# Kernel tuning notes

Hardware: AMD Instinct MI355X
Metric: run time of the kernel (lower is better)

The kernel has to match this reference:

```python
import jax, jax.numpy as jnp
import numpy as np
import math

B, S, D = 16, 2048, 128
MASK_SENTINEL = -100

def setup_inputs() -> dict:
    key = jax.random.key(0)
    k1, k2, k3, k4 = jax.random.split(key, 4)
    value = jax.random.normal(k1, (B, S, D), dtype=jnp.float32)
    key_t = jax.random.normal(k2, (B, S, D), dtype=jnp.float32)
    query = jax.random.normal(k3, (B, S, D), dtype=jnp.float32)
    # mask uses -100 as the "masked out" sentinel, anything else is kept.
    bits = jax.random.randint(k4, (B, S, S), 0, 2, dtype=jnp.int32)
    mask = jnp.where(bits == 0, jnp.int32(MASK_SENTINEL), jnp.int32(0))
    return {"value": value, "key": key_t, "query": query, "mask": mask}

def reference(value, key, query, mask):
    # scores: [B, Sq, Sk]
    scale = 1.0 / math.sqrt(query.shape[-1])
    scores = jnp.einsum("bqd,bkd->bqk", query, key) * scale
    min_val = jnp.finfo(scores.dtype).min
    masked = jnp.where(mask == MASK_SENTINEL, min_val, scores)
    attn = jax.nn.softmax(masked, axis=-1)
    return jnp.einsum("bqk,bkd->bqd", attn, value)
```

## Files before the change

kernel.cpp:

```cpp
#include <hip/hip_runtime.h>
#include <hip/hip_bf16.h>

#define BATCH 16
#define SEQ   2048
#define DIM   128
#define QBLK  64
#define KVBLK 64
#define NT    (SEQ / KVBLK)
#define PPAD  72
#define L2E   1.4426950408889634f
#define THR   8.0f
#define MSENT -100

typedef __attribute__((ext_vector_type(8))) short bf16x8;
typedef __attribute__((ext_vector_type(4))) float f32x4;
typedef __attribute__((ext_vector_type(4))) int   i32x4;
typedef __attribute__((ext_vector_type(4))) unsigned u32x4;

__device__ __forceinline__ unsigned short f2bf(float f) {
  union { float f; unsigned u; } v; v.f = f;
  return (unsigned short)((v.u + 0x7FFFu + ((v.u >> 16) & 1u)) >> 16);
}
__device__ __forceinline__ unsigned packbf(float a, float b) {
  return ((unsigned)f2bf(b) << 16) | (unsigned)f2bf(a);
}

__global__ __launch_bounds__(256) void cvt_k(const float* __restrict__ K,
                                             short* __restrict__ Kb) {
  const size_t i = ((size_t)blockIdx.x * 256 + threadIdx.x) * 8;
  f32x4 a = __builtin_nontemporal_load((const f32x4*)(K + i));
  f32x4 b = __builtin_nontemporal_load((const f32x4*)(K + i + 4));
  u32x4 o = { packbf(a[0], a[1]), packbf(a[2], a[3]),
              packbf(b[0], b[1]), packbf(b[2], b[3]) };
  *(u32x4*)(Kb + i) = o;
}

__global__ __launch_bounds__(256) void cvt_vt(const float* __restrict__ V,
                                              short* __restrict__ Vt) {
  __shared__ unsigned t32[64][65];
  const int tid = threadIdx.x;
  const int b  = blockIdx.x >> 5;
  const int s0 = (blockIdx.x & 31) * 64;
  #pragma unroll
  for (int it = 0; it < 8; ++it) {
    const int idx = tid + it * 256;
    const int r = idx >> 5, c4 = idx & 31;
    f32x4 x = __builtin_nontemporal_load(
        (const f32x4*)(V + ((size_t)b * SEQ + s0 + r) * DIM + c4 * 4));
    t32[r][c4 * 2]     = packbf(x[0], x[1]);
    t32[r][c4 * 2 + 1] = packbf(x[2], x[3]);
  }
  __syncthreads();
  const int d = tid >> 1, sh = tid & 1;
  unsigned short outv[32];
  #pragma unroll
  for (int j = 0; j < 32; ++j) {
    const unsigned u = t32[sh * 32 + j][d >> 1];
    outv[j] = (d & 1) ? (unsigned short)(u >> 16) : (unsigned short)(u & 0xffff);
  }
  short* op = Vt + ((size_t)b * DIM + d) * SEQ + s0 + sh * 32;
  #pragma unroll
  for (int q = 0; q < 4; ++q) {
    bf16x8 y;
    #pragma unroll
    for (int j = 0; j < 8; ++j) y[j] = (short)outv[q * 8 + j];
    *(bf16x8*)(op + q * 8) = y;
  }
}

__device__ __forceinline__ void gload16(const void* g, void* l) {
  __builtin_amdgcn_global_load_lds(
      (const __attribute__((address_space(1))) unsigned*)g,
      (__attribute__((address_space(3))) unsigned*)l, 16, 0, 0);
}

__device__ __forceinline__ void stage_k(const char* __restrict__ Kb2,
                                        int k0, int w, int l, void* kbuf) {
  #pragma unroll
  for (int it = 0; it < 4; ++it) {
    const int ch = w * 4 + it;
    const int r  = ch * 4 + (l >> 4);
    const int sg = (l & 15) ^ (r & 15);
    gload16(Kb2 + (size_t)(k0 + r) * 256 + sg * 16, (char*)kbuf + ch * 1024);
  }
}
__device__ __forceinline__ void stage_v(const char* __restrict__ Vtb2,
                                        int k0, int w, int l, void* vbuf) {
  #pragma unroll
  for (int it = 0; it < 4; ++it) {
    const int ch = w * 4 + it;
    const int d2 = ch * 4 + (l >> 4);
    const int Su = (l & 15) ^ (d2 & 15);
    const int d  = 2 * d2 + (Su >> 3);
    const int m  = Su & 7;
    gload16(Vtb2 + (size_t)d * (SEQ * 2) + (size_t)k0 * 2 + m * 16,
            (char*)vbuf + ch * 1024);
  }
}

#define TILE_BODY(T, PAR, SA, SB, MA, MB)                                      \
  {                                                                            \
    if ((T) + 2 < NT) stage_k(Kb2, ((T) + 2) * KVBLK, w, l, lds_k[(PAR)]);     \
    if ((T) + 1 < NT) stage_v(Vtb2, ((T) + 1) * KVBLK, w, l, lds_v[(PAR) ^ 1]);\
    __builtin_amdgcn_sched_barrier(0);                                         \
                  \
    _Pragma("unroll") for (int sub = 0; sub < 4; ++sub)                        \
        _Pragma("unroll") for (int i = 0; i < 4; ++i)                          \
            if (MA[sub][i] == MSENT) SA[sub][i] = -1e30f;                      \
    {                                                                          \
      float tm = -1e30f;                                                       \
      _Pragma("unroll") for (int sub = 0; sub < 4; ++sub)                      \
          _Pragma("unroll") for (int i = 0; i < 4; ++i)                        \
              tm = fmaxf(tm, SA[sub][i]);                                      \
      tm = fmaxf(tm, __shfl_xor(tm, 16));                                      \
      tm = fmaxf(tm, __shfl_xor(tm, 32));                                      \
      if (__any(tm > mrow + THR)) {                                            \
        const float mnew = fmaxf(mrow, tm);                                    \
        const float al = __builtin_amdgcn_exp2f((mrow - mnew) * L2E);          \
        mrow = mnew; lsum *= al;                                               \
        float av[4];                                                           \
        _Pragma("unroll") for (int i = 0; i < 4; ++i)                          \
            av[i] = __shfl(al, 4 * g + i);                                     \
        _Pragma("unroll") for (int t8 = 0; t8 < 8; ++t8)                       \
            _Pragma("unroll") for (int i = 0; i < 4; ++i)                      \
                acc[t8][i] *= av[i];                                           \
      }                                                                        \
    }                                                                          \
           \
    if ((T) + 1 < NT) {                                                        \
      _Pragma("unroll") for (int sub = 0; sub < 4; ++sub)                      \
          MB[sub] = __builtin_nontemporal_load(                                \
              (const i32x4*)(Mr + ((T) + 1) * KVBLK + 16 * sub + 4 * g));      \
    }                                                                          \
               \
    if ((T) + 1 < NT) {                                                        \
      const char* kb_ = (const char*)lds_k[(PAR) ^ 1];                         \
      _Pragma("unroll") for (int sub = 0; sub < 4; ++sub)                      \
          SB[sub] = (f32x4){0.f, 0.f, 0.f, 0.f};                               \
      __builtin_amdgcn_s_setprio(1);                                           \
      _Pragma("unroll") for (int kk = 0; kk < 4; ++kk) {                       \
        const int cb = (64 * kk + 16 * g) ^ (lr << 4);                         \
        _Pragma("unroll") for (int sub = 0; sub < 4; ++sub) {                  \
          bf16x8 kb = *(const bf16x8*)(kb_ + (sub * 16 + lr) * 256 + cb);      \
          SB[sub] = __builtin_amdgcn_mfma_f32_16x16x32_bf16(kb, qa[kk],        \
                                                            SB[sub], 0, 0, 0); \
        }                                                                      \
      }                                                                        \
      __builtin_amdgcn_s_setprio(0);                                           \
    }                                                                          \
                               \
    {                                                                          \
      unsigned* prow = (unsigned*)&lds_p[w][lr * PPAD];                        \
      _Pragma("unroll") for (int sub = 0; sub < 4; ++sub) {                    \
        const float p0 = __builtin_amdgcn_exp2f((SA[sub][0] - mrow) * L2E);    \
        const float p1 = __builtin_amdgcn_exp2f((SA[sub][1] - mrow) * L2E);    \
        const float p2 = __builtin_amdgcn_exp2f((SA[sub][2] - mrow) * L2E);    \
        const float p3 = __builtin_amdgcn_exp2f((SA[sub][3] - mrow) * L2E);    \
        lsum += (p0 + p1) + (p2 + p3);                                         \
        prow[8 * sub + 2 * g]     = packbf(p0, p1);                            \
        prow[8 * sub + 2 * g + 1] = packbf(p2, p3);                            \
      }                                                                        \
      bf16x8 pa0 = *(const bf16x8*)&lds_p[w][lr * PPAD + g * 8];               \
      bf16x8 pa1 = *(const bf16x8*)&lds_p[w][lr * PPAD + 32 + g * 8];          \
      const char* vb_ = (const char*)lds_v[(PAR)];                             \
      __builtin_amdgcn_s_setprio(1);                                           \
      _Pragma("unroll") for (int t8 = 0; t8 < 8; ++t8) {                       \
        const int d2 = 8 * t8 + (lr >> 1);                                     \
        const int S0 = (((lr & 1) * 8 + 0 + g) ^ (d2 & 15)) * 16;              \
        const int S1 = (((lr & 1) * 8 + 4 + g) ^ (d2 & 15)) * 16;              \
        bf16x8 v0 = *(const bf16x8*)(vb_ + d2 * 256 + S0);                     \
        acc[t8] = __builtin_amdgcn_mfma_f32_16x16x32_bf16(pa0, v0, acc[t8],    \
                                                          0, 0, 0);            \
        bf16x8 v1 = *(const bf16x8*)(vb_ + d2 * 256 + S1);                     \
        acc[t8] = __builtin_amdgcn_mfma_f32_16x16x32_bf16(pa1, v1, acc[t8],    \
                                                          0, 0, 0);            \
      }                                                                        \
      __builtin_amdgcn_s_setprio(0);                                           \
    }                                                                          \
    if ((T) + 1 < NT) __syncthreads();                                         \
  }

__global__ __launch_bounds__(256, 2) void attn_fwd(
    const short* __restrict__ Kbf, const short* __restrict__ Vt,
    const float* __restrict__ Qg, const int* __restrict__ Mg,
    float* __restrict__ Og) {
  __shared__ short lds_k[2][KVBLK * DIM];
  __shared__ short lds_v[2][DIM * KVBLK];
  __shared__ short lds_p[4][16 * PPAD];

  const int tid = threadIdx.x;
  const int w = tid >> 6, l = tid & 63, g = l >> 4, lr = l & 15;

  const int blk = blockIdx.x;
  const int swz = (blk & 7) * 64 + (blk >> 3);
  const int b   = swz >> 5;
  const int q0  = (swz & 31) * QBLK;

  const float scale = 0.08838834764831845f;

  const char* Kb2  = (const char*)(Kbf + (size_t)b * SEQ * DIM);
  const char* Vtb2 = (const char*)(Vt  + (size_t)b * DIM * SEQ);
  const int*  Mr   = Mg + (size_t)b * SEQ * SEQ + (size_t)(q0 + w * 16 + lr) * SEQ;

  stage_k(Kb2, 0,     w, l, lds_k[0]);
  stage_k(Kb2, KVBLK, w, l, lds_k[1]);
  stage_v(Vtb2, 0,    w, l, lds_v[0]);
  __builtin_amdgcn_sched_barrier(0);
  i32x4 mA[4], mB[4];
  #pragma unroll
  for (int sub = 0; sub < 4; ++sub)
    mA[sub] = __builtin_nontemporal_load((const i32x4*)(Mr + 16 * sub + 4 * g));

  bf16x8 qa[4];
  {
    const float* qbase = Qg + ((size_t)b * SEQ + (size_t)(q0 + w * 16 + lr)) * DIM + g * 8;
    #pragma unroll
    for (int kk = 0; kk < 4; ++kk) {
      f32x4 x0 = *(const f32x4*)(qbase + kk * 32);
      f32x4 x1 = *(const f32x4*)(qbase + kk * 32 + 4);
      bf16x8 f;
      #pragma unroll
      for (int j = 0; j < 4; ++j) {
        f[j]     = (short)f2bf(x0[j] * scale);
        f[j + 4] = (short)f2bf(x1[j] * scale);
      }
      qa[kk] = f;
    }
  }

  f32x4 acc[8];
  #pragma unroll
  for (int t = 0; t < 8; ++t) acc[t] = (f32x4){0.f, 0.f, 0.f, 0.f};
  float mrow = -1e30f, lsum = 0.f;

  __syncthreads();

  f32x4 sA[4], sB[4];
  #pragma unroll
  for (int sub = 0; sub < 4; ++sub) sA[sub] = (f32x4){0.f, 0.f, 0.f, 0.f};
  {
    const char* kb_ = (const char*)lds_k[0];
    #pragma unroll
    for (int kk = 0; kk < 4; ++kk) {
      const int cb = (64 * kk + 16 * g) ^ (lr << 4);
      #pragma unroll
      for (int sub = 0; sub < 4; ++sub) {
        bf16x8 kb = *(const bf16x8*)(kb_ + (sub * 16 + lr) * 256 + cb);
        sA[sub] = __builtin_amdgcn_mfma_f32_16x16x32_bf16(kb, qa[kk], sA[sub], 0, 0, 0);
      }
    }
  }
  __syncthreads();

  for (int t = 0; t < NT; t += 2) {
    TILE_BODY(t,     0, sA, sB, mA, mB);
    TILE_BODY(t + 1, 1, sB, sA, mB, mA);
  }

  lsum += __shfl_xor(lsum, 16);
  lsum += __shfl_xor(lsum, 32);
  const float rden = 1.f / lsum;
  float rdv[4];
  #pragma unroll
  for (int i = 0; i < 4; ++i) rdv[i] = __shfl(rden, 4 * g + i);
  float* ob = Og + ((size_t)b * SEQ + (size_t)(q0 + w * 16)) * DIM;
  #pragma unroll
  for (int t8 = 0; t8 < 8; ++t8)
    #pragma unroll
    for (int i = 0; i < 4; ++i)
      ob[(4 * g + i) * DIM + 16 * t8 + lr] = acc[t8][i] * rdv[i];
}

extern "C" void kernel_launch(void* const* d_in, const int* in_sizes, int n_in,
                              void* d_out, int out_size, void* d_ws, size_t ws_size,
                              hipStream_t stream) {
  (void)in_sizes; (void)n_in; (void)out_size; (void)ws_size;
  const float* Vg = (const float*)d_in[0];
  const float* Kg = (const float*)d_in[1];
  const float* Qg = (const float*)d_in[2];
  const int*   Mg = (const int*)d_in[3];
  float* Og = (float*)d_out;

  short* Kbf = (short*)d_ws;
  short* Vt  = Kbf + (size_t)BATCH * SEQ * DIM;
  cvt_k<<<dim3(BATCH * SEQ * DIM / (8 * 256)), 256, 0, stream>>>(Kg, Kbf);
  cvt_vt<<<dim3(BATCH * (SEQ / 64)), 256, 0, stream>>>(Vg, Vt);
  attn_fwd<<<dim3(BATCH * (SEQ / QBLK)), 256, 0, stream>>>(Kbf, Vt, Qg, Mg, Og);
}
```

Measured before the change: 108.4 us.

## Load V tiles directly from global into registers instead of staging through LDS

Removes the LDS double-buffer for V. Each wave now reads its V^T fragments straight from global memory into 16 bf16x8 registers at the start of each tile, and the mask prefetch moves up next to those loads. This drops the LDS traffic and LDS footprint for V, which may allow higher occupancy. The costs are 64 extra VGPRs per thread, redundant global/L2 reads of the same V tile by all four waves, and V load latency that is no longer prefetched a tile ahead.

```diff
diff --git a/kernel.cpp b/kernel.cpp
--- a/kernel.cpp
+++ b/kernel.cpp
@@ -84,24 +84,21 @@
     gload16(Kb2 + (size_t)(k0 + r) * 256 + sg * 16, (char*)kbuf + ch * 1024);
   }
 }
-__device__ __forceinline__ void stage_v(const char* __restrict__ Vtb2,
-                                        int k0, int w, int l, void* vbuf) {
-  #pragma unroll
-  for (int it = 0; it < 4; ++it) {
-    const int ch = w * 4 + it;
-    const int d2 = ch * 4 + (l >> 4);
-    const int Su = (l & 15) ^ (d2 & 15);
-    const int d  = 2 * d2 + (Su >> 3);
-    const int m  = Su & 7;
-    gload16(Vtb2 + (size_t)d * (SEQ * 2) + (size_t)k0 * 2 + m * 16,
-            (char*)vbuf + ch * 1024);
-  }
-}
 
 #define TILE_BODY(T, PAR, SA, SB, MA, MB)                                      \
   {                                                                            \
     if ((T) + 2 < NT) stage_k(Kb2, ((T) + 2) * KVBLK, w, l, lds_k[(PAR)]);     \
-    if ((T) + 1 < NT) stage_v(Vtb2, ((T) + 1) * KVBLK, w, l, lds_v[(PAR) ^ 1]);\
+                                            \
+    _Pragma("unroll") for (int t8 = 0; t8 < 8; ++t8) {                         \
+      const short* vrow = VtS + (size_t)(16 * t8 + lr) * SEQ + (T) * KVBLK;    \
+      vr[2 * t8]     = *(const bf16x8*)(vrow + g * 8);                         \
+      vr[2 * t8 + 1] = *(const bf16x8*)(vrow + 32 + g * 8);                    \
+    }                                                                          \
+    if ((T) + 1 < NT) {                                                        \
+      _Pragma("unroll") for (int sub = 0; sub < 4; ++sub)                      \
+          MB[sub] = __builtin_nontemporal_load(                                \
+              (const i32x4*)(Mr + ((T) + 1) * KVBLK + 16 * sub + 4 * g));      \
+    }                                                                          \
     __builtin_amdgcn_sched_barrier(0);                                         \
                   \
     _Pragma("unroll") for (int sub = 0; sub < 4; ++sub)                        \
@@ -126,12 +123,6 @@
                 acc[t8][i] *= av[i];                                           \
       }                                                                        \
     }                                                                          \
-           \
-    if ((T) + 1 < NT) {                                                        \
-      _Pragma("unroll") for (int sub = 0; sub < 4; ++sub)                      \
-          MB[sub] = __builtin_nontemporal_load(                                \
-              (const i32x4*)(Mr + ((T) + 1) * KVBLK + 16 * sub + 4 * g));      \
-    }                                                                          \
                \
     if ((T) + 1 < NT) {                                                        \
       const char* kb_ = (const char*)lds_k[(PAR) ^ 1];                         \
@@ -148,7 +139,7 @@
       }                                                                        \
       __builtin_amdgcn_s_setprio(0);                                           \
     }                                                                          \
-                               \
+                       \
     {                                                                          \
       unsigned* prow = (unsigned*)&lds_p[w][lr * PPAD];                        \
       _Pragma("unroll") for (int sub = 0; sub < 4; ++sub) {                    \
@@ -162,18 +153,12 @@
       }                                                                        \
       bf16x8 pa0 = *(const bf16x8*)&lds_p[w][lr * PPAD + g * 8];               \
       bf16x8 pa1 = *(const bf16x8*)&lds_p[w][lr * PPAD + 32 + g * 8];          \
-      const char* vb_ = (const char*)lds_v[(PAR)];                             \
       __builtin_amdgcn_s_setprio(1);                                           \
       _Pragma("unroll") for (int t8 = 0; t8 < 8; ++t8) {                       \
-        const int d2 = 8 * t8 + (lr >> 1);                                     \
-        const int S0 = (((lr & 1) * 8 + 0 + g) ^ (d2 & 15)) * 16;              \
-        const int S1 = (((lr & 1) * 8 + 4 + g) ^ (d2 & 15)) * 16;              \
-        bf16x8 v0 = *(const bf16x8*)(vb_ + d2 * 256 + S0);                     \
-        acc[t8] = __builtin_amdgcn_mfma_f32_16x16x32_bf16(pa0, v0, acc[t8],    \
-                                                          0, 0, 0);            \
-        bf16x8 v1 = *(const bf16x8*)(vb_ + d2 * 256 + S1);                     \
-        acc[t8] = __builtin_amdgcn_mfma_f32_16x16x32_bf16(pa1, v1, acc[t8],    \
-                                                          0, 0, 0);            \
+        acc[t8] = __builtin_amdgcn_mfma_f32_16x16x32_bf16(pa0, vr[2 * t8],     \
+                                                          acc[t8], 0, 0, 0);   \
+        acc[t8] = __builtin_amdgcn_mfma_f32_16x16x32_bf16(pa1, vr[2 * t8 + 1], \
+                                                          acc[t8], 0, 0, 0);   \
       }                                                                        \
       __builtin_amdgcn_s_setprio(0);                                           \
     }                                                                          \
@@ -185,7 +170,6 @@
     const float* __restrict__ Qg, const int* __restrict__ Mg,
     float* __restrict__ Og) {
   __shared__ short lds_k[2][KVBLK * DIM];
-  __shared__ short lds_v[2][DIM * KVBLK];
   __shared__ short lds_p[4][16 * PPAD];
 
   const int tid = threadIdx.x;
@@ -198,13 +182,12 @@
 
   const float scale = 0.08838834764831845f;
 
-  const char* Kb2  = (const char*)(Kbf + (size_t)b * SEQ * DIM);
-  const char* Vtb2 = (const char*)(Vt  + (size_t)b * DIM * SEQ);
-  const int*  Mr   = Mg + (size_t)b * SEQ * SEQ + (size_t)(q0 + w * 16 + lr) * SEQ;
+  const char*  Kb2 = (const char*)(Kbf + (size_t)b * SEQ * DIM);
+  const short* VtS = Vt + (size_t)b * DIM * SEQ;
+  const int*   Mr  = Mg + (size_t)b * SEQ * SEQ + (size_t)(q0 + w * 16 + lr) * SEQ;
 
   stage_k(Kb2, 0,     w, l, lds_k[0]);
   stage_k(Kb2, KVBLK, w, l, lds_k[1]);
-  stage_v(Vtb2, 0,    w, l, lds_v[0]);
   __builtin_amdgcn_sched_barrier(0);
   i32x4 mA[4], mB[4];
   #pragma unroll
@@ -232,6 +215,7 @@
   #pragma unroll
   for (int t = 0; t < 8; ++t) acc[t] = (f32x4){0.f, 0.f, 0.f, 0.f};
   float mrow = -1e30f, lsum = 0.f;
+  bf16x8 vr[16];
 
   __syncthreads();
 
```

Result: slower. 190.5 us (+75.8%).
